# Kernel optimization log

Hardware: AMD Instinct MI355X
Metric: run time of the kernel (lower is better)

## Reference

```python
import jax, jax.numpy as jnp
import numpy as np

P = 16; RES = 224; D = 768; L = 12; H = 12; OUT = 512
NP1 = NP2 = RES // P          # 14x14 patches
NTOK = NP1 * NP2 + 1          # 197 tokens (cls + patches)
STD = 5.0                     # gaussian_std for naclip
EPS = 1e-5


def _ln(x, w, b):
    x32 = x.astype(jnp.float32)
    m = x32.mean(-1, keepdims=True)
    v = ((x32 - m) ** 2).mean(-1, keepdims=True)
    return (((x32 - m) * jax.lax.rsqrt(v + EPS)) * w + b).astype(x.dtype)


def _quick_gelu(x):
    return x * jax.nn.sigmoid(1.702 * x)


def _gaussian_addition():
    # VisionTransformer.gaussian_window + get_attention_addition, done analytically:
    # addition[i*NP2+j, k*NP2+l] = window[k-i+NP1-1, l-j+NP2-1]
    w1, w2 = 2 * NP1 - 1, 2 * NP2 - 1
    c = 1.0 / (STD * np.sqrt(2.0))
    k1 = (-(w1 - 1) / 2.0 + np.arange(w1)) * c
    k2 = (-(w2 - 1) / 2.0 + np.arange(w2)) * c
    window = np.exp(-(k1[:, None] ** 2 + k2[None, :] ** 2))
    r = np.arange(NP1)[None, :] - np.arange(NP1)[:, None] + (NP1 - 1)  # [i,k]
    cc = np.arange(NP2)[None, :] - np.arange(NP2)[:, None] + (NP2 - 1)  # [j,l]
    A = window[r[:, None, :, None], cc[None, :, None, :]]  # (NP1,NP2,NP1,NP2)
    A = A.reshape(NP1 * NP2, NP1 * NP2)
    full = np.zeros((NTOK, NTOK), dtype=np.float32)
    full[1:, 1:] = A  # zero row/col for cls token
    return jnp.asarray(full)


def _mha_vanilla(x, wi, bi, wo, bo):
    B, N, _ = x.shape
    hd = D // H
    qkv = x @ wi.T + bi                      # [B,N,3D]
    q, k, v = jnp.split(qkv, 3, axis=-1)
    q = q.reshape(B, N, H, hd); k = k.reshape(B, N, H, hd); v = v.reshape(B, N, H, hd)
    a = jnp.einsum('bqhd,bkhd->bhqk', q, k) * (hd ** -0.5)
    a = jax.nn.softmax(a, axis=-1)
    o = jnp.einsum('bhqk,bkhd->bqhd', a, v).reshape(B, N, D)
    return o @ wo.T + bo


def _mha_naclip(x, wi, bi, wo, bo, addition):
    B, N, _ = x.shape
    hd = D // H
    qkv = x @ wi.T + bi
    _, k, v = jnp.split(qkv, 3, axis=-1)
    k = k.reshape(B, N, H, hd); v = v.reshape(B, N, H, hd)
    a = jnp.einsum('bqhd,bkhd->bhqk', k, k) * (hd ** -0.5) + addition[None, None]
    a = jax.nn.softmax(a, axis=-1)
    o = jnp.einsum('bhqk,bkhd->bqhd', a, v).reshape(B, N, D)
    return o @ wo.T + bo


def _mlp(x, fw, fb, pw, pb):
    return _quick_gelu(x @ fw.T + fb) @ pw.T + pb


def setup_inputs() -> dict:
    key = jax.random.key(0)
    ks = jax.random.split(key, 16)
    s = D ** -0.5
    rn = lambda k, shape, sc=0.02: jax.random.normal(k, shape, jnp.float32) * sc
    return {
        'x': jax.random.normal(ks[0], (32, 3, RES, RES), jnp.float32),
        'conv1_w': rn(ks[1], (D, 3, P, P)),
        'class_embedding': rn(ks[2], (D,), s),
        'pos_embedding': rn(ks[3], (NTOK, D), s),
        'ln_pre_w': jnp.ones((D,)), 'ln_pre_b': jnp.zeros((D,)),
        'in_proj_w': rn(ks[4], (L, 3 * D, D)), 'in_proj_b': rn(ks[5], (L, 3 * D)),
        'out_proj_w': rn(ks[6], (L, D, D)), 'out_proj_b': rn(ks[7], (L, D)),
        'ln1_w': jnp.ones((L, D)), 'ln1_b': jnp.zeros((L, D)),
        'ln2_w': jnp.ones((L, D)), 'ln2_b': jnp.zeros((L, D)),
        'fc_w': rn(ks[8], (L, 4 * D, D)), 'fc_b': rn(ks[9], (L, 4 * D)),
        'cproj_w': rn(ks[10], (L, D, 4 * D)), 'cproj_b': rn(ks[11], (L, D)),
        'ln_post_w': jnp.ones((D,)), 'ln_post_b': jnp.zeros((D,)),
        'proj': rn(ks[12], (D, OUT), s),
    }


def reference(x, conv1_w, class_embedding, pos_embedding, ln_pre_w, ln_pre_b,
              in_proj_w, in_proj_b, out_proj_w, out_proj_b, ln1_w, ln1_b,
              ln2_w, ln2_b, fc_w, fc_b, cproj_w, cproj_b, ln_post_w, ln_post_b, proj):
    B = x.shape[0]
    # patch embed
    h = jax.lax.conv_general_dilated(x, conv1_w, (P, P), 'VALID',
                                     dimension_numbers=('NCHW', 'OIHW', 'NCHW'))
    h = h.reshape(B, D, NP1 * NP2).transpose(0, 2, 1)           # [B,196,D]
    cls = jnp.broadcast_to(class_embedding, (B, 1, D))
    h = jnp.concatenate([cls, h], axis=1) + pos_embedding        # [B,197,D]
    h = _ln(h, ln_pre_w, ln_pre_b)
    addition = _gaussian_addition()
    # first L-1 blocks: vanilla attention
    for i in range(L - 1):
        h = h + _mha_vanilla(_ln(h, ln1_w[i], ln1_b[i]), in_proj_w[i], in_proj_b[i],
                             out_proj_w[i], out_proj_b[i])
        h = h + _mlp(_ln(h, ln2_w[i], ln2_b[i]), fc_w[i], fc_b[i], cproj_w[i], cproj_b[i])
    # last block: naclip key-key attention with gaussian addition (arch='vanilla')
    i = L - 1
    reduced = _mha_naclip(_ln(h, ln1_w[i], ln1_b[i]), in_proj_w[i], in_proj_b[i],
                          out_proj_w[i], out_proj_b[i], addition)
    final = h + reduced
    final = final + _mlp(_ln(final, ln2_w[i], ln2_b[i]), fc_w[i], fc_b[i], cproj_w[i], cproj_b[i])
    return _ln(final, ln_post_w, ln_post_b) @ proj               # [B,197,OUT]
```

## Files before the change

### kernel.cpp

```cpp
#include <hip/hip_runtime.h>
#include <hip/hip_bf16.h>
#include <math.h>

#define BATCH 32
#define NTOK  197
#define NPATCH 196
#define DMODEL 768
#define NLAYER 12
#define NHEAD 12
#define HDIM  64
#define ROWS  (BATCH*NTOK)
#define CROWS (BATCH*NPATCH)
#define DFF   3072
#define DQKV  2304
#define DOUT  512
#define NBH   (BATCH*NHEAD)

#define WOFF_IN   ((size_t)0)
#define WOFF_OUT  ((size_t)(DQKV*DMODEL))
#define WOFF_FC   (WOFF_OUT + (size_t)(DMODEL*DMODEL))
#define WOFF_CP   (WOFF_FC + (size_t)(DFF*DMODEL))
#define WTOT      (WOFF_CP + (size_t)(DMODEL*DFF))

#define WS_H    ((size_t)0)
#define WS_QKVB (WS_H + (size_t)ROWS*DMODEL)
#define WS_GB   (WS_QKVB + (size_t)ROWS*DQKV/2)
#define WS_TB   (WS_GB + (size_t)ROWS*DFF/2)
#define WS_WL   (WS_TB + (size_t)ROWS*DMODEL/2)
#define WS_PTS  (WS_WL + WTOT/2)
#define WS_ADD  (WS_PTS + (size_t)DOUT*DMODEL/2)

typedef unsigned short ushort_t;
typedef __attribute__((ext_vector_type(8))) short bf16x8;
typedef __attribute__((ext_vector_type(4))) float f32x4;

__device__ inline ushort_t bf16rn(float x) {
    uint32_t u = __builtin_bit_cast(uint32_t, x);
    uint32_t r = (u + 0x7FFFu + ((u >> 16) & 1u)) >> 16;
    return (ushort_t)r;
}

#define GLL(src, dst) __builtin_amdgcn_global_load_lds( \
    (const __attribute__((address_space(1))) void*)(src), \
    (__attribute__((address_space(3))) void*)(dst), 16, 0, 0)


__global__ void im2col_bf16_k(const float* __restrict__ x, ushort_t* __restrict__ out) {
    int idx = blockIdx.x * 256 + threadIdx.x;
    if (idx >= CROWS * DMODEL / 4) return;
    int r  = idx / (DMODEL / 4);
    int k4 = (idx - r * (DMODEL / 4)) * 4;
    int b = r / NPATCH, p = r - b * NPATCH;
    int py = p / 14, px = p - py * 14;
    int c = k4 >> 8, rem = k4 & 255, i = rem >> 4, j = rem & 15;
    const float* xp = x + (((size_t)(b * 3 + c) * 224) + py * 16 + i) * 224 + px * 16 + j;
    float4 v = *(const float4*)xp;
    ushort4 hv = {bf16rn(v.x), bf16rn(v.y), bf16rn(v.z), bf16rn(v.w)};
    *(ushort4*)(out + (size_t)r * DMODEL + k4) = hv;
}

__global__ void cvt_w_k(const float* __restrict__ W, ushort_t* __restrict__ out, int NK) {
    int idx = (blockIdx.x * 256 + threadIdx.x) * 4;
    if (idx >= NK) return;
    float4 v = *(const float4*)(W + idx);
    ushort4 hv = {bf16rn(v.x), bf16rn(v.y), bf16rn(v.z), bf16rn(v.w)};
    *(ushort4*)(out + idx) = hv;
}

__global__ void cvt_layer_k(const float* __restrict__ inW, const float* __restrict__ outW,
                            const float* __restrict__ fcW, const float* __restrict__ cpW,
                            ushort_t* __restrict__ wl) {
    size_t idx = ((size_t)blockIdx.x * 256 + threadIdx.x) * 4;
    if (idx >= WTOT) return;
    const float* src; size_t off;
    if (idx < WOFF_OUT)      { src = inW;  off = idx; }
    else if (idx < WOFF_FC)  { src = outW; off = idx - WOFF_OUT; }
    else if (idx < WOFF_CP)  { src = fcW;  off = idx - WOFF_FC; }
    else                     { src = cpW;  off = idx - WOFF_CP; }
    float4 v = *(const float4*)(src + off);
    ushort4 hv = {bf16rn(v.x), bf16rn(v.y), bf16rn(v.z), bf16rn(v.w)};
    *(ushort4*)(wl + idx) = hv;
}

__global__ void cvt_pT_k(const float* __restrict__ proj, ushort_t* __restrict__ out) {
    int idx = blockIdx.x * 256 + threadIdx.x;
    if (idx >= DOUT * DMODEL) return;
    int n = idx / DMODEL, k = idx - n * DMODEL;
    out[(size_t)n * DMODEL + k] = bf16rn(proj[(size_t)k * DOUT + n]);
}

__global__ void gauss_k(float* __restrict__ add) {
    int idx = blockIdx.x * 256 + threadIdx.x;
    if (idx >= NTOK * NTOK) return;
    int i = idx / NTOK, j = idx - i * NTOK;
    float v = 0.f;
    if (i > 0 && j > 0) {
        int p = i - 1, q = j - 1;
        int di = q / 14 - p / 14;
        int dj = q % 14 - p % 14;
        v = expf(-(float)(di * di + dj * dj) * 0.02f);
    }
    add[idx] = v;
}

__global__ __launch_bounds__(256) void embed_lnpre_k(const float* __restrict__ conv,
                                                     const float* __restrict__ cls,
                                                     const float* __restrict__ pos,
                                                     const float* __restrict__ w,
                                                     const float* __restrict__ b,
                                                     float* __restrict__ h) {
    int row = blockIdx.x, tid = threadIdx.x;
    int bb = row / NTOK, tok = row - bb * NTOK;
    float e[3];
    #pragma unroll
    for (int c = 0; c < 3; ++c) {
        int d = tid + c * 256;
        float v = (tok == 0) ? cls[d] : conv[((size_t)(bb * NPATCH + tok - 1)) * DMODEL + d];
        e[c] = v + pos[(size_t)tok * DMODEL + d];
    }
    float s = e[0] + e[1] + e[2];
    float s2 = e[0]*e[0] + e[1]*e[1] + e[2]*e[2];
    for (int o = 32; o > 0; o >>= 1) { s += __shfl_down(s, o); s2 += __shfl_down(s2, o); }
    __shared__ float red[8];
    int wid = tid >> 6;
    if ((tid & 63) == 0) { red[wid] = s; red[4 + wid] = s2; }
    __syncthreads();
    s  = red[0] + red[1] + red[2] + red[3];
    s2 = red[4] + red[5] + red[6] + red[7];
    float mean = s * (1.0f / 768.0f);
    float var  = s2 * (1.0f / 768.0f) - mean * mean;
    float rinv = rsqrtf(var + 1e-5f);
    float* o_ = h + (size_t)row * DMODEL;
    #pragma unroll
    for (int c = 0; c < 3; ++c) {
        int d = tid + c * 256;
        o_[d] = (e[c] - mean) * rinv * w[d] + b[d];
    }
}

__global__ __launch_bounds__(256) void ln768_bf16_k(const float* __restrict__ in, ushort_t* __restrict__ out,
                                                    const float* __restrict__ w, const float* __restrict__ b) {
    int row = blockIdx.x, tid = threadIdx.x;
    const float* x = in + (size_t)row * DMODEL;
    float v0 = x[tid], v1 = x[tid + 256], v2 = x[tid + 512];
    float s = v0 + v1 + v2;
    float s2 = v0 * v0 + v1 * v1 + v2 * v2;
    for (int o = 32; o > 0; o >>= 1) { s += __shfl_down(s, o); s2 += __shfl_down(s2, o); }
    __shared__ float red[8];
    int wid = tid >> 6;
    if ((tid & 63) == 0) { red[wid] = s; red[4 + wid] = s2; }
    __syncthreads();
    s  = red[0] + red[1] + red[2] + red[3];
    s2 = red[4] + red[5] + red[6] + red[7];
    float mean = s * (1.0f / 768.0f);
    float var  = s2 * (1.0f / 768.0f) - mean * mean;
    float rinv = rsqrtf(var + 1e-5f);
    ushort_t* o_ = out + (size_t)row * DMODEL;
    o_[tid]       = bf16rn((v0 - mean) * rinv * w[tid]       + b[tid]);
    o_[tid + 256] = bf16rn((v1 - mean) * rinv * w[tid + 256] + b[tid + 256]);
    o_[tid + 512] = bf16rn((v2 - mean) * rinv * w[tid + 512] + b[tid + 512]);
}

template<int DEPTH>
__global__ __launch_bounds__(256) void gemm_mfma_k(
    const ushort_t* __restrict__ A, const ushort_t* __restrict__ W,
    const float* __restrict__ bias, float* __restrict__ C, ushort_t* __restrict__ OS,
    int M, int N, int K, int mode)
{
    __shared__ ushort_t As[DEPTH][128][32];
    __shared__ ushort_t Bs[DEPTH][128][32];
    int tid = threadIdx.x;
    int lane = tid & 63;
    int wave = tid >> 6;
    int wm = wave >> 1, wn = wave & 1;
    int m0 = blockIdx.x * 128, n0 = blockIdx.y * 128;

    int klen = K / gridDim.z;
    int kbeg = blockIdx.z * klen;
    int nt = klen / 32;

    f32x4 acc[4][4];
    #pragma unroll
    for (int i = 0; i < 4; ++i)
        #pragma unroll
        for (int j = 0; j < 4; ++j)
            acc[i][j] = (f32x4){0.f, 0.f, 0.f, 0.f};

    int srow = tid >> 2;
    int skq  = (((tid & 3) ^ ((tid >> 3) & 3)) * 8);
    int ar0 = m0 + srow;      if (ar0 > M - 1) ar0 = M - 1;
    int ar1 = m0 + srow + 64; if (ar1 > M - 1) ar1 = M - 1;
    const ushort_t* Ap0 = A + (size_t)ar0 * K + kbeg + skq;
    const ushort_t* Ap1 = A + (size_t)ar1 * K + kbeg + skq;
    const ushort_t* Wp0 = W + (size_t)(n0 + srow) * K + kbeg + skq;
    const ushort_t* Wp1 = W + (size_t)(n0 + srow + 64) * K + kbeg + skq;
    char* ldsA = (char*)As + tid * 16;
    char* ldsB = (char*)Bs + tid * 16;

    int fr = lane & 15, fq = lane >> 4;
    int rsl = (fq ^ ((fr >> 1) & 3)) * 8;

    #define STAGE(buf_, ko_) do {                         \
        GLL(Ap0 + (ko_), ldsA + (buf_) * 8192);           \
        GLL(Ap1 + (ko_), ldsA + (buf_) * 8192 + 4096);    \
        GLL(Wp0 + (ko_), ldsB + (buf_) * 8192);           \
        GLL(Wp1 + (ko_), ldsB + (buf_) * 8192 + 4096);    \
    } while (0)

    STAGE(0, 0);
    if (nt > 1) STAGE(1, 32);

    for (int t = 0; t < nt; ++t) {
        int cur = t % DEPTH;
        if (t + 1 < nt) asm volatile("s_waitcnt vmcnt(4)" ::: "memory");
        else            asm volatile("s_waitcnt vmcnt(0)" ::: "memory");
        __builtin_amdgcn_s_barrier();
        if (t + DEPTH - 1 < nt) STAGE((t + DEPTH - 1) % DEPTH, (size_t)(t + DEPTH - 1) * 32);
        bf16x8 a[4], b[4];
        #pragma unroll
        for (int fm = 0; fm < 4; ++fm)
            a[fm] = *(const bf16x8*)&As[cur][wm * 64 + fm * 16 + fr][rsl];
        #pragma unroll
        for (int fn = 0; fn < 4; ++fn)
            b[fn] = *(const bf16x8*)&Bs[cur][wn * 64 + fn * 16 + fr][rsl];
        #pragma unroll
        for (int fm = 0; fm < 4; ++fm)
            #pragma unroll
            for (int fn = 0; fn < 4; ++fn)
                acc[fm][fn] = __builtin_amdgcn_mfma_f32_16x16x32_bf16(a[fm], b[fn], acc[fm][fn], 0, 0, 0);
    }
    #undef STAGE

    #pragma unroll
    for (int fn = 0; fn < 4; ++fn) {
        int ccol = n0 + wn * 64 + fn * 16 + fr;
        float bv = bias ? bias[ccol] : 0.f;
        if (mode == 3 && blockIdx.z != 0) bv = 0.f;
        #pragma unroll
        for (int fm = 0; fm < 4; ++fm) {
            int crow0 = m0 + wm * 64 + fm * 16 + fq * 4;
            #pragma unroll
            for (int j = 0; j < 4; ++j) {
                int row = crow0 + j;
                if (row < M) {
                    float v = acc[fm][fn][j] + bv;
                    if (mode == 0) {
                        C[(size_t)row * N + ccol] = v;
                    } else if (mode == 3) {
                        atomicAdd(&C[(size_t)row * N + ccol], v);
                    } else if (mode == 4) {
                        OS[(size_t)row * N + ccol] = bf16rn(v);
                    } else {
                        v = v / (1.0f + expf(-1.702f * v));
                        OS[(size_t)row * N + ccol] = bf16rn(v);
                    }
                }
            }
        }
    }
}

__global__ __launch_bounds__(512, 4) void attn_fused_k(
    const ushort_t* __restrict__ qkvb, ushort_t* __restrict__ out,
    const float* __restrict__ addition, int qoff)
{
    __shared__ ushort_t Ks[208][72];
    __shared__ ushort_t Vt[64][232];
    __shared__ ushort_t Pb[8][2][16][40];
    int tid = threadIdx.x;
    int bh = blockIdx.x;
    int b = bh / NHEAD, hh = bh - b * NHEAD;
    const ushort_t* base = qkvb + (size_t)b * NTOK * DQKV + hh * HDIM;

    int lane = tid & 63, wave = tid >> 6;
    int fr = lane & 15, fq = lane >> 4;
    int qt = blockIdx.y * 8 + wave;

    bf16x8 qf0, qf1;
    if (qt < 13) {
        int qrow = qt * 16 + fr; if (qrow > NTOK - 1) qrow = NTOK - 1;
        const ushort_t* qp = base + (size_t)qrow * DQKV + qoff + fq * 8;
        qf0 = *(const bf16x8*)qp;
        qf1 = *(const bf16x8*)(qp + 32);
    }

    {
        int tt = tid >> 4, dq = tid & 15;
        #pragma unroll
        for (int pass = 0; pass < 7; ++pass) {
            int t = pass * 32 + tt;
            if (t < 208) {
                ushort4 kv = {0, 0, 0, 0}, vv = {0, 0, 0, 0};
                if (t < NTOK) {
                    kv = *(const ushort4*)(base + (size_t)t * DQKV + DMODEL + dq * 4);
                    vv = *(const ushort4*)(base + (size_t)t * DQKV + 2 * DMODEL + dq * 4);
                }
                *(ushort4*)&Ks[t][dq * 4] = kv;
                Vt[dq * 4 + 0][t] = vv.x;
                Vt[dq * 4 + 1][t] = vv.y;
                Vt[dq * 4 + 2][t] = vv.z;
                Vt[dq * 4 + 3][t] = vv.w;
            }
        }
        for (int z = tid; z < 64 * 24; z += 512) Vt[z / 24][208 + z % 24] = 0;
    }
    __syncthreads();

    if (qt < 13) {
        int i0 = qt * 16;
        int irow = i0 + fr; if (irow > NTOK - 1) irow = NTOK - 1;

        f32x4 s[13];
        #pragma unroll
        for (int jt = 0; jt < 13; ++jt) {
            bf16x8 k0 = *(const bf16x8*)&Ks[jt * 16 + fr][fq * 8];
            bf16x8 k1 = *(const bf16x8*)&Ks[jt * 16 + fr][32 + fq * 8];
            f32x4 a = {0.f, 0.f, 0.f, 0.f};
            a = __builtin_amdgcn_mfma_f32_16x16x32_bf16(k0, qf0, a, 0, 0, 0);
            a = __builtin_amdgcn_mfma_f32_16x16x32_bf16(k1, qf1, a, 0, 0, 0);
            s[jt] = a;
        }

        float mx = -1e30f;
        #pragma unroll
        for (int jt = 0; jt < 13; ++jt) {
            int jb = jt * 16 + fq * 4;
            #pragma unroll
            for (int jj = 0; jj < 4; ++jj) {
                int j = jb + jj;
                float v = s[jt][jj] * 0.125f;
                if (addition) v += addition[irow * NTOK + (j < NTOK ? j : NTOK - 1)];
                if (j >= NTOK) v = -1e30f;
                s[jt][jj] = v;
                mx = fmaxf(mx, v);
            }
        }
        mx = fmaxf(mx, __shfl_xor(mx, 16));
        mx = fmaxf(mx, __shfl_xor(mx, 32));
        float sum = 0.f;
        #pragma unroll
        for (int jt = 0; jt < 13; ++jt)
            #pragma unroll
            for (int jj = 0; jj < 4; ++jj) {
                float e = __expf(s[jt][jj] - mx);
                s[jt][jj] = e;
                sum += e;
            }
        sum += __shfl_xor(sum, 16);
        sum += __shfl_xor(sum, 32);
        float inv = 1.0f / sum;

        f32x4 o4[4];
        #pragma unroll
        for (int dt = 0; dt < 4; ++dt) o4[dt] = (f32x4){0.f, 0.f, 0.f, 0.f};

        #define WRITE_P(st_, buf_) do {                                              \
            int jA = 2 * (st_), jB = jA + 1;                                         \
            ushort4 wa = {bf16rn(s[jA][0] * inv), bf16rn(s[jA][1] * inv),            \
                          bf16rn(s[jA][2] * inv), bf16rn(s[jA][3] * inv)};           \
            ushort4 wb = {0, 0, 0, 0};                                               \
            if (jB < 13) wb = (ushort4){bf16rn(s[jB][0] * inv), bf16rn(s[jB][1] * inv), \
                                        bf16rn(s[jB][2] * inv), bf16rn(s[jB][3] * inv)}; \
            *(ushort4*)&Pb[wave][buf_][fr][fq * 4] = wa;                             \
            *(ushort4*)&Pb[wave][buf_][fr][16 + fq * 4] = wb;                        \
        } while (0)

        WRITE_P(0, 0);
        for (int st = 0; st < 7; ++st) {
            asm volatile("s_waitcnt lgkmcnt(0)" ::: "memory");
            bf16x8 pa = *(const bf16x8*)&Pb[wave][st & 1][fr][fq * 8];
            bf16x8 vf0 = *(const bf16x8*)&Vt[0 * 16 + fr][st * 32 + fq * 8];
            bf16x8 vf1 = *(const bf16x8*)&Vt[1 * 16 + fr][st * 32 + fq * 8];
            bf16x8 vf2 = *(const bf16x8*)&Vt[2 * 16 + fr][st * 32 + fq * 8];
            bf16x8 vf3 = *(const bf16x8*)&Vt[3 * 16 + fr][st * 32 + fq * 8];
            if (st < 6) WRITE_P(st + 1, (st + 1) & 1);
            o4[0] = __builtin_amdgcn_mfma_f32_16x16x32_bf16(pa, vf0, o4[0], 0, 0, 0);
            o4[1] = __builtin_amdgcn_mfma_f32_16x16x32_bf16(pa, vf1, o4[1], 0, 0, 0);
            o4[2] = __builtin_amdgcn_mfma_f32_16x16x32_bf16(pa, vf2, o4[2], 0, 0, 0);
            o4[3] = __builtin_amdgcn_mfma_f32_16x16x32_bf16(pa, vf3, o4[3], 0, 0, 0);
        }
        #undef WRITE_P

        #pragma unroll
        for (int jj = 0; jj < 4; ++jj) {
            int ir = i0 + fq * 4 + jj;
            if (ir < NTOK) {
                ushort_t* op = out + ((size_t)(b * NTOK + ir)) * DMODEL + hh * HDIM + fr;
                #pragma unroll
                for (int dt = 0; dt < 4; ++dt)
                    op[dt * 16] = bf16rn(o4[dt][jj]);
            }
        }
    }
}

extern "C" void kernel_launch(void* const* d_in, const int* in_sizes, int n_in,
                              void* d_out, int out_size, void* d_ws, size_t ws_size,
                              hipStream_t stream) {
    const float* x        = (const float*)d_in[0];
    const float* conv1_w  = (const float*)d_in[1];
    const float* cls      = (const float*)d_in[2];
    const float* pos      = (const float*)d_in[3];
    const float* ln_pre_w = (const float*)d_in[4];
    const float* ln_pre_b = (const float*)d_in[5];
    const float* in_proj_w  = (const float*)d_in[6];
    const float* in_proj_b  = (const float*)d_in[7];
    const float* out_proj_w = (const float*)d_in[8];
    const float* out_proj_b = (const float*)d_in[9];
    const float* ln1_w = (const float*)d_in[10];
    const float* ln1_b = (const float*)d_in[11];
    const float* ln2_w = (const float*)d_in[12];
    const float* ln2_b = (const float*)d_in[13];
    const float* fc_w  = (const float*)d_in[14];
    const float* fc_b  = (const float*)d_in[15];
    const float* cproj_w = (const float*)d_in[16];
    const float* cproj_b = (const float*)d_in[17];
    const float* ln_post_w = (const float*)d_in[18];
    const float* ln_post_b = (const float*)d_in[19];
    const float* proj = (const float*)d_in[20];
    float* out = (float*)d_out;

    float* ws   = (float*)d_ws;
    float* h    = ws + WS_H;
    float* ctmp = ws + WS_QKVB;
    ushort_t* qkvb = (ushort_t*)(ws + WS_QKVB);
    ushort_t* gb   = (ushort_t*)(ws + WS_GB);
    ushort_t* tb   = (ushort_t*)(ws + WS_TB);
    ushort_t* wl   = (ushort_t*)(ws + WS_WL);
    ushort_t* pTs  = (ushort_t*)(ws + WS_PTS);
    float* add  = ws + WS_ADD;

    ushort_t* convw = gb;

    im2col_bf16_k<<<(CROWS * DMODEL / 4 + 255) / 256, 256, 0, stream>>>(x, tb);
    cvt_w_k<<<(DMODEL * DMODEL / 4 + 255) / 256, 256, 0, stream>>>(conv1_w, convw, DMODEL * DMODEL);
    hipMemsetAsync(ctmp, 0, (size_t)CROWS * DMODEL * sizeof(float), stream);
    gemm_mfma_k<3><<<dim3((CROWS + 127) / 128, DMODEL / 128, 2), 256, 0, stream>>>(
        tb, convw, nullptr, ctmp, nullptr, CROWS, DMODEL, DMODEL, 3);
    embed_lnpre_k<<<ROWS, 256, 0, stream>>>(ctmp, cls, pos, ln_pre_w, ln_pre_b, h);
    gauss_k<<<(NTOK * NTOK + 255) / 256, 256, 0, stream>>>(add);
    cvt_pT_k<<<(DOUT * DMODEL + 255) / 256, 256, 0, stream>>>(proj, pTs);

    const int GY = (ROWS + 127) / 128;
    for (int l = 0; l < NLAYER; ++l) {
        cvt_layer_k<<<(int)(WTOT / 4 / 256), 256, 0, stream>>>(
            in_proj_w + (size_t)l * DQKV * DMODEL, out_proj_w + (size_t)l * DMODEL * DMODEL,
            fc_w + (size_t)l * DFF * DMODEL, cproj_w + (size_t)l * DMODEL * DFF, wl);
        ln768_bf16_k<<<ROWS, 256, 0, stream>>>(h, tb, ln1_w + l * DMODEL, ln1_b + l * DMODEL);
        gemm_mfma_k<3><<<dim3(GY, DQKV / 128), 256, 0, stream>>>(
            tb, wl + WOFF_IN, in_proj_b + (size_t)l * DQKV, nullptr, qkvb, ROWS, DQKV, DMODEL, 4);
        bool nac = (l == NLAYER - 1);
        attn_fused_k<<<dim3(NBH, 2), 512, 0, stream>>>(qkvb, tb, nac ? add : nullptr, nac ? DMODEL : 0);
        gemm_mfma_k<3><<<dim3(GY, DMODEL / 128, 2), 256, 0, stream>>>(
            tb, wl + WOFF_OUT, out_proj_b + (size_t)l * DMODEL, h, nullptr, ROWS, DMODEL, DMODEL, 3);
        ln768_bf16_k<<<ROWS, 256, 0, stream>>>(h, tb, ln2_w + l * DMODEL, ln2_b + l * DMODEL);
        gemm_mfma_k<3><<<dim3(GY, DFF / 128), 256, 0, stream>>>(
            tb, wl + WOFF_FC, fc_b + (size_t)l * DFF, nullptr, gb, ROWS, DFF, DMODEL, 1);
        gemm_mfma_k<3><<<dim3(GY, DMODEL / 128, 2), 256, 0, stream>>>(
            gb, wl + WOFF_CP, cproj_b + (size_t)l * DMODEL, h, nullptr, ROWS, DMODEL, DFF, 3);
    }

    ln768_bf16_k<<<ROWS, 256, 0, stream>>>(h, tb, ln_post_w, ln_post_b);
    hipMemsetAsync(out, 0, (size_t)out_size * sizeof(float), stream);
    gemm_mfma_k<3><<<dim3(GY, DOUT / 128, 2), 256, 0, stream>>>(
        tb, pTs, nullptr, out, nullptr, ROWS, DOUT, DMODEL, 3);
}
```

Baseline: 3.476 ms.

## Overlap next-layer weight conversion with QKV GEMM and swizzle tiles across XCDs

Removes the per-layer standalone weight fp32->bf16 conversion kernel. Extra workgroups appended to the QKV GEMM launch now convert the next layer's weights into a double-buffered workspace slot, so the conversion overlaps with GEMM work. It also remaps the linear workgroup id so consecutive tiles land on the same XCD for better L2 locality, and replaces modulo buffer indexing with incrementing counters. The workspace for converted weights doubles, and only two extra blocks per row-tile column do the conversion, which could make those blocks a tail straggler.

```diff
diff --git a/kernel.cpp b/kernel.cpp
--- a/kernel.cpp
+++ b/kernel.cpp
@@ -27,7 +27,7 @@
 #define WS_GB   (WS_QKVB + (size_t)ROWS*DQKV/2)
 #define WS_TB   (WS_GB + (size_t)ROWS*DFF/2)
 #define WS_WL   (WS_TB + (size_t)ROWS*DMODEL/2)
-#define WS_PTS  (WS_WL + WTOT/2)
+#define WS_PTS  (WS_WL + WTOT)
 #define WS_ADD  (WS_PTS + (size_t)DOUT*DMODEL/2)
 
 typedef unsigned short ushort_t;
@@ -165,18 +165,55 @@
 __global__ __launch_bounds__(256) void gemm_mfma_k(
     const ushort_t* __restrict__ A, const ushort_t* __restrict__ W,
     const float* __restrict__ bias, float* __restrict__ C, ushort_t* __restrict__ OS,
-    int M, int N, int K, int mode)
+    int M, int N, int K, int mode,
+    const float* __restrict__ c0, const float* __restrict__ c1,
+    const float* __restrict__ c2, const float* __restrict__ c3, ushort_t* __restrict__ cdst)
 {
     __shared__ ushort_t As[DEPTH][128][32];
     __shared__ ushort_t Bs[DEPTH][128][32];
     int tid = threadIdx.x;
+
+    int nm = (M + 127) >> 7;
+    int nn = N >> 7;
+    int nz = gridDim.z;
+    int normal = nm * nn * nz;
+    int lin = blockIdx.x + gridDim.x * (blockIdx.y + gridDim.y * blockIdx.z);
+    int nwg = gridDim.x * gridDim.y * gridDim.z;
+
+    if (lin >= normal) {
+        int cvtb = nwg - normal;
+        size_t i = (size_t)(lin - normal) * 256 + tid;
+        size_t stride = (size_t)cvtb * 256;
+        for (; i < WTOT / 4; i += stride) {
+            size_t idx = i * 4;
+            const float* src; size_t off;
+            if (idx < WOFF_OUT)      { src = c0; off = idx; }
+            else if (idx < WOFF_FC)  { src = c1; off = idx - WOFF_OUT; }
+            else if (idx < WOFF_CP)  { src = c2; off = idx - WOFF_FC; }
+            else                     { src = c3; off = idx - WOFF_CP; }
+            float4 v = *(const float4*)(src + off);
+            ushort4 hv = {bf16rn(v.x), bf16rn(v.y), bf16rn(v.z), bf16rn(v.w)};
+            *(ushort4*)(cdst + idx) = hv;
+        }
+        return;
+    }
+
+    int q = normal >> 3, rr = normal & 7;
+    int xcd = lin & 7, kk = lin >> 3;
+    int w = (xcd < rr) ? (xcd * (q + 1) + kk) : (rr * (q + 1) + (xcd - rr) * q + kk);
+    int pm = nn * nz;
+    int mb = w / pm;
+    int rest = w - mb * pm;
+    int nb = rest / nz;
+    int zb = rest - nb * nz;
+    int m0 = mb * 128, n0 = nb * 128;
+
     int lane = tid & 63;
     int wave = tid >> 6;
     int wm = wave >> 1, wn = wave & 1;
-    int m0 = blockIdx.x * 128, n0 = blockIdx.y * 128;
-
-    int klen = K / gridDim.z;
-    int kbeg = blockIdx.z * klen;
+
+    int klen = K / nz;
+    int kbeg = zb * klen;
     int nt = klen / 32;
 
     f32x4 acc[4][4];
@@ -210,12 +247,12 @@
     STAGE(0, 0);
     if (nt > 1) STAGE(1, 32);
 
+    int cur = 0, pre = (DEPTH - 1) % DEPTH;
     for (int t = 0; t < nt; ++t) {
-        int cur = t % DEPTH;
         if (t + 1 < nt) asm volatile("s_waitcnt vmcnt(4)" ::: "memory");
         else            asm volatile("s_waitcnt vmcnt(0)" ::: "memory");
         __builtin_amdgcn_s_barrier();
-        if (t + DEPTH - 1 < nt) STAGE((t + DEPTH - 1) % DEPTH, (size_t)(t + DEPTH - 1) * 32);
+        if (t + DEPTH - 1 < nt) STAGE(pre, (size_t)(t + DEPTH - 1) * 32);
         bf16x8 a[4], b[4];
         #pragma unroll
         for (int fm = 0; fm < 4; ++fm)
@@ -228,6 +265,8 @@
             #pragma unroll
             for (int fn = 0; fn < 4; ++fn)
                 acc[fm][fn] = __builtin_amdgcn_mfma_f32_16x16x32_bf16(a[fm], b[fn], acc[fm][fn], 0, 0, 0);
+        cur = (cur + 1 == DEPTH) ? 0 : cur + 1;
+        pre = (pre + 1 == DEPTH) ? 0 : pre + 1;
     }
     #undef STAGE
 
@@ -235,7 +274,7 @@
     for (int fn = 0; fn < 4; ++fn) {
         int ccol = n0 + wn * 64 + fn * 16 + fr;
         float bv = bias ? bias[ccol] : 0.f;
-        if (mode == 3 && blockIdx.z != 0) bv = 0.f;
+        if (mode == 3 && zb != 0) bv = 0.f;
         #pragma unroll
         for (int fm = 0; fm < 4; ++fm) {
             int crow0 = m0 + wm * 64 + fm * 16 + fq * 4;
@@ -393,6 +432,8 @@
         }
     }
 }
+
+#define NOCVT nullptr, nullptr, nullptr, nullptr, nullptr
 
 extern "C" void kernel_launch(void* const* d_in, const int* in_sizes, int n_in,
                               void* d_out, int out_size, void* d_ws, size_t ws_size,
@@ -435,33 +476,41 @@
     im2col_bf16_k<<<(CROWS * DMODEL / 4 + 255) / 256, 256, 0, stream>>>(x, tb);
     cvt_w_k<<<(DMODEL * DMODEL / 4 + 255) / 256, 256, 0, stream>>>(conv1_w, convw, DMODEL * DMODEL);
     hipMemsetAsync(ctmp, 0, (size_t)CROWS * DMODEL * sizeof(float), stream);
-    gemm_mfma_k<3><<<dim3((CROWS + 127) / 128, DMODEL / 128, 2), 256, 0, stream>>>(
-        tb, convw, nullptr, ctmp, nullptr, CROWS, DMODEL, DMODEL, 3);
+    gemm_mfma_k<3><<<dim3(49, 6, 2), 256, 0, stream>>>(
+        tb, convw, nullptr, ctmp, nullptr, CROWS, DMODEL, DMODEL, 3, NOCVT);
     embed_lnpre_k<<<ROWS, 256, 0, stream>>>(ctmp, cls, pos, ln_pre_w, ln_pre_b, h);
     gauss_k<<<(NTOK * NTOK + 255) / 256, 256, 0, stream>>>(add);
     cvt_pT_k<<<(DOUT * DMODEL + 255) / 256, 256, 0, stream>>>(proj, pTs);
+    cvt_layer_k<<<(int)(WTOT / 4 / 256), 256, 0, stream>>>(in_proj_w, out_proj_w, fc_w, cproj_w, wl);
 
     const int GY = (ROWS + 127) / 128;
     for (int l = 0; l < NLAYER; ++l) {
-        cvt_layer_k<<<(int)(WTOT / 4 / 256), 256, 0, stream>>>(
-            in_proj_w + (size_t)l * DQKV * DMODEL, out_proj_w + (size_t)l * DMODEL * DMODEL,
-            fc_w + (size_t)l * DFF * DMODEL, cproj_w + (size_t)l * DMODEL * DFF, wl);
+        ushort_t* wlp = wl + (size_t)(l & 1) * WTOT;
         ln768_bf16_k<<<ROWS, 256, 0, stream>>>(h, tb, ln1_w + l * DMODEL, ln1_b + l * DMODEL);
-        gemm_mfma_k<3><<<dim3(GY, DQKV / 128), 256, 0, stream>>>(
-            tb, wl + WOFF_IN, in_proj_b + (size_t)l * DQKV, nullptr, qkvb, ROWS, DQKV, DMODEL, 4);
+        if (l + 1 < NLAYER) {
+            int l2 = l + 1;
+            gemm_mfma_k<3><<<dim3(GY, DQKV / 128 + 2), 256, 0, stream>>>(
+                tb, wlp + WOFF_IN, in_proj_b + (size_t)l * DQKV, nullptr, qkvb, ROWS, DQKV, DMODEL, 4,
+                in_proj_w + (size_t)l2 * DQKV * DMODEL, out_proj_w + (size_t)l2 * DMODEL * DMODEL,
+                fc_w + (size_t)l2 * DFF * DMODEL, cproj_w + (size_t)l2 * DMODEL * DFF,
+                wl + (size_t)(l2 & 1) * WTOT);
+        } else {
+            gemm_mfma_k<3><<<dim3(GY, DQKV / 128), 256, 0, stream>>>(
+                tb, wlp + WOFF_IN, in_proj_b + (size_t)l * DQKV, nullptr, qkvb, ROWS, DQKV, DMODEL, 4, NOCVT);
+        }
         bool nac = (l == NLAYER - 1);
         attn_fused_k<<<dim3(NBH, 2), 512, 0, stream>>>(qkvb, tb, nac ? add : nullptr, nac ? DMODEL : 0);
         gemm_mfma_k<3><<<dim3(GY, DMODEL / 128, 2), 256, 0, stream>>>(
-            tb, wl + WOFF_OUT, out_proj_b + (size_t)l * DMODEL, h, nullptr, ROWS, DMODEL, DMODEL, 3);
+            tb, wlp + WOFF_OUT, out_proj_b + (size_t)l * DMODEL, h, nullptr, ROWS, DMODEL, DMODEL, 3, NOCVT);
         ln768_bf16_k<<<ROWS, 256, 0, stream>>>(h, tb, ln2_w + l * DMODEL, ln2_b + l * DMODEL);
         gemm_mfma_k<3><<<dim3(GY, DFF / 128), 256, 0, stream>>>(
-            tb, wl + WOFF_FC, fc_b + (size_t)l * DFF, nullptr, gb, ROWS, DFF, DMODEL, 1);
+            tb, wlp + WOFF_FC, fc_b + (size_t)l * DFF, nullptr, gb, ROWS, DFF, DMODEL, 1, NOCVT);
         gemm_mfma_k<3><<<dim3(GY, DMODEL / 128, 2), 256, 0, stream>>>(
-            gb, wl + WOFF_CP, cproj_b + (size_t)l * DMODEL, h, nullptr, ROWS, DMODEL, DFF, 3);
+            gb, wlp + WOFF_CP, cproj_b + (size_t)l * DMODEL, h, nullptr, ROWS, DMODEL, DFF, 3, NOCVT);
     }
 
     ln768_bf16_k<<<ROWS, 256, 0, stream>>>(h, tb, ln_post_w, ln_post_b);
     hipMemsetAsync(out, 0, (size_t)out_size * sizeof(float), stream);
     gemm_mfma_k<3><<<dim3(GY, DOUT / 128, 2), 256, 0, stream>>>(
-        tb, pTs, nullptr, out, nullptr, ROWS, DOUT, DMODEL, 3);
-}
+        tb, pTs, nullptr, out, nullptr, ROWS, DOUT, DMODEL, 3, NOCVT);
+}
```

New measurement: 3.601 ms. +3.6%, slower.
